# Optimization experiments

Measured on AMD Instinct MI355X. Metric: run time of the kernel, lower is better.

## Reference

```python
import jax, jax.numpy as jnp
import numpy as np

B, N, FIN, FOUT = 8, 4096, 64, 64
NEG_SLOPE = 0.01  # torch LeakyReLU default


def setup_inputs() -> dict:
    key = jax.random.key(0)
    k1, k2, k3, k4, k5 = jax.random.split(key, 5)
    inp = jax.random.normal(k1, (B, N, FIN), dtype=jnp.float32)
    adj = jax.random.randint(k2, (N, N), 0, 2, dtype=jnp.int32)
    W_w = jax.random.normal(k3, (FOUT, FIN), dtype=jnp.float32) * (1.0 / np.sqrt(FIN))
    W_b = jax.random.normal(k4, (FOUT,), dtype=jnp.float32) * 0.01
    a = jax.random.normal(k5, (2 * FOUT, N), dtype=jnp.float32) * (1.414 / np.sqrt(2 * FOUT + N))
    return {"inp": inp, "adj": adj, "W_w": W_w, "W_b": W_b, "a": a}


def reference(inp, adj, W_w, W_b, a):
    # h = W(inp); h[:, 0, :] = 0
    h = jnp.einsum('bnf,of->bno', inp, W_w) + W_b          # [B, N, F]
    h = h.at[:, 0, :].set(0.0)

    # Original loop: for i in 1..N-1:
    #   ac = a[:, i]  (shape [2F, 1])
    #   index = where(adj[1:, i] > 0)  -> 0-based, used to index h directly (bug preserved)
    #   s_i = h[:, i, :] @ ac[:F] + sum_j h[:, index, :] @ ac[F:]   (scalar per batch)
    #   attention[:, i, :] = s_i broadcast over all columns
    # Empty-index case equals the general case since an empty neighbor sum is 0.
    mask = (adj[1:, :] > 0).astype(h.dtype)                # [N-1, N]
    neigh = jnp.einsum('ji,bjf->bif', mask, h[:, :N - 1, :])  # [B, N, F]
    s = (jnp.einsum('bif,fi->bi', h, a[:FOUT]) +
         jnp.einsum('bif,fi->bi', neigh, a[FOUT:]))        # [B, N]
    s = s.at[:, 0].set(0.0)                                # attention row 0 stays zero

    # h_prime = attention @ h, with attention[b,i,j] = s[b,i] for all j
    hsum = h.sum(axis=1)                                   # [B, F]
    h_prime = s[:, :, None] * hsum[:, None, :]             # [B, N, F]
    return jnp.where(h_prime >= 0, h_prime, NEG_SLOPE * h_prime)
```

## Files before the change

kernel.cpp:

```cpp
#include <hip/hip_runtime.h>
#include <hip/hip_bf16.h>

#define NN 4096

typedef unsigned short u16;
typedef __attribute__((ext_vector_type(8))) short short8;
typedef __attribute__((ext_vector_type(4))) float f32x4;
typedef __attribute__((ext_vector_type(4))) unsigned short u16x4;
typedef __attribute__((ext_vector_type(8))) unsigned short u16x8;
typedef __attribute__((ext_vector_type(4))) int i32x4;

typedef const void __attribute__((address_space(1)))* gas_t;
typedef void __attribute__((address_space(3)))* las_t;

__device__ __forceinline__ u16 f2bf(float x) {
  unsigned u = __float_as_uint(x);
  return (u16)((u + 0x7FFFu + ((u >> 16) & 1)) >> 16);
}

__global__ __launch_bounds__(256) void k_maskT(const int* __restrict__ adj, u16* __restrict__ maskT) {
  __shared__ __align__(16) u16 tile[128 * 132];
  const int i0 = blockIdx.x * 128, j0 = blockIdx.y * 128;
  const int t = threadIdx.x;
  const int jr = t >> 5;
  const int il = t & 31;
#pragma unroll
  for (int pass = 0; pass < 16; ++pass) {
    const int jl = pass * 8 + jr;
    const int j = j0 + jl;
    u16 q[4] = {0, 0, 0, 0};
    if (j < NN - 1) {
      i32x4 av = *reinterpret_cast<const i32x4*>(&adj[(size_t)(j + 1) * NN + i0 + il * 4]);
      q[0] = av.x > 0 ? 0x3F80 : 0;
      q[1] = av.y > 0 ? 0x3F80 : 0;
      q[2] = av.z > 0 ? 0x3F80 : 0;
      q[3] = av.w > 0 ? 0x3F80 : 0;
    }
    const int pb = il ^ (jl >> 2);
    *reinterpret_cast<u16x4*>(&tile[jl * 132 + pb * 4]) = *reinterpret_cast<u16x4*>(q);
  }
  __syncthreads();
#pragma unroll
  for (int pass = 0; pass < 16; ++pass) {
    const int ir = pass * 8 + jr;
    const int ci = ir >> 2, io = ir & 3;
    u16 o[4];
#pragma unroll
    for (int d = 0; d < 4; ++d) {
      const int r = il * 4 + d;
      o[d] = tile[r * 132 + ((ci ^ il) << 2) + io];
    }
    *reinterpret_cast<u16x4*>(&maskT[(size_t)(i0 + ir) * NN + j0 + il * 4]) =
        *reinterpret_cast<u16x4*>(o);
  }
}

__global__ __launch_bounds__(256) void k_h(const float* __restrict__ inp, const float* __restrict__ Ww,
                                           const float* __restrict__ Wb, float* __restrict__ h,
                                           u16* __restrict__ h2t, float* __restrict__ hsum) {
  __shared__ __align__(16) u16 lA[128 * 64];
  __shared__ __align__(16) u16 lW[64 * 64];
  const int t = threadIdx.x, lane = t & 63, w = t >> 6;
  const int bid = blockIdx.x;
  const int b = bid >> 5;
  const size_t row0 = (size_t)bid * 128;
  {
    const int o = t >> 2, k0 = (t & 3) * 16;
    const float* src = &Ww[o * 64 + k0];
    u16 tmp[16];
#pragma unroll
    for (int e = 0; e < 16; ++e) tmp[e] = f2bf(src[e]);
    const int swz = (o & 7) * 8;
#pragma unroll
    for (int v = 0; v < 2; ++v)
      *reinterpret_cast<u16x8*>(&lW[o * 64 + ((k0 + v * 8) ^ swz)]) = *reinterpret_cast<u16x8*>(&tmp[v * 8]);
  }
  {
    const int r = t >> 1, k0 = (t & 1) * 32;
    const float* src = &inp[(row0 + r) * 64 + k0];
    u16 tmp[32];
#pragma unroll
    for (int e = 0; e < 32; ++e) tmp[e] = f2bf(src[e]);
    const int swz = (r & 7) * 8;
#pragma unroll
    for (int v = 0; v < 4; ++v)
      *reinterpret_cast<u16x8*>(&lA[r * 64 + ((k0 + v * 8) ^ swz)]) = *reinterpret_cast<u16x8*>(&tmp[v * 8]);
  }
  __syncthreads();
  f32x4 acc[2][4] = {};
#pragma unroll
  for (int ks = 0; ks < 2; ++ks) {
    const int kk = ks * 32 + (lane >> 4) * 8;
    short8 af[2], bf[4];
#pragma unroll
    for (int m = 0; m < 2; ++m) {
      const int row = w * 32 + m * 16 + (lane & 15);
      af[m] = *reinterpret_cast<const short8*>(&lA[row * 64 + (kk ^ ((row & 7) * 8))]);
    }
#pragma unroll
    for (int n = 0; n < 4; ++n) {
      const int o = n * 16 + (lane & 15);
      bf[n] = *reinterpret_cast<const short8*>(&lW[o * 64 + (kk ^ ((o & 7) * 8))]);
    }
#pragma unroll
    for (int m = 0; m < 2; ++m)
#pragma unroll
      for (int n = 0; n < 4; ++n)
        acc[m][n] = __builtin_amdgcn_mfma_f32_16x16x32_bf16(af[m], bf[n], acc[m][n], 0, 0, 0);
  }
  const int f0 = lane & 15;
  const int rsub = (lane >> 4) * 4;
  float wb[4];
#pragma unroll
  for (int n = 0; n < 4; ++n) wb[n] = Wb[n * 16 + f0];
  const int nloc_base = (bid & 31) * 128;
  float ps[4] = {0.f, 0.f, 0.f, 0.f};
#pragma unroll
  for (int m = 0; m < 2; ++m) {
    const int rl = w * 32 + m * 16 + rsub;
#pragma unroll
    for (int n = 0; n < 4; ++n) {
      u16 hb[4];
#pragma unroll
      for (int r = 0; r < 4; ++r) {
        float v = acc[m][n][r] + wb[n];
        if (nloc_base + rl + r == 0) v = 0.f;
        h[(row0 + rl + r) * 64 + n * 16 + f0] = v;
        hb[r] = f2bf(v);
        ps[n] += v;
      }
      *reinterpret_cast<u16x4*>(&h2t[(size_t)(b * 64 + n * 16 + f0) * NN + nloc_base + rl]) =
          *reinterpret_cast<u16x4*>(&hb[0]);
    }
  }
#pragma unroll
  for (int n = 0; n < 4; ++n) {
    float v = ps[n];
    v += __shfl_xor(v, 16);
    v += __shfl_xor(v, 32);
    if (lane < 16) atomicAdd(&hsum[b * 64 + n * 16 + f0], v);
  }
}

__global__ __launch_bounds__(256, 2) void k_gemm(const u16* __restrict__ A, const u16* __restrict__ Bm,
                                                 const float* __restrict__ a, float* __restrict__ s) {
  __shared__ __align__(16) u16 lA0[128 * 64], lA1[128 * 64];
  __shared__ __align__(16) u16 lB0[128 * 64], lB1[128 * 64];
  const int sid = blockIdx.x;
  const int wgid = (sid & 7) * 64 + (sid >> 3);
  const int c0 = (wgid & 3) * 128;
  const int i0 = ((wgid >> 2) & 31) * 128;
  const int z = wgid >> 7;
  const int t = threadIdx.x, lane = t & 63, w = t >> 6;
  const int wr = w >> 1, wc = w & 1;

  const int srow = lane >> 3;
  const int sk = ((lane & 7) ^ srow) * 8;
  const size_t kbase = (size_t)z * 1024;
  const u16* gA = A + (size_t)(i0 + w * 32 + srow) * NN + kbase + sk;
  const u16* gB = Bm + (size_t)(c0 + w * 32 + srow) * NN + kbase + sk;

#define STAGE_K(dstA, dstB, kt)                                                              \
  do {                                                                                       \
    _Pragma("unroll") for (int c = 0; c < 4; ++c) {                                          \
      __builtin_amdgcn_global_load_lds((gas_t)(gA + (size_t)(8 * c) * NN + (kt)),            \
                                       (las_t)((dstA) + (w * 32 + 8 * c) * 128 + lane * 16), \
                                       16, 0, 0);                                            \
      __builtin_amdgcn_global_load_lds((gas_t)(gB + (size_t)(8 * c) * NN + (kt)),            \
                                       (las_t)((dstB) + (w * 32 + 8 * c) * 128 + lane * 16), \
                                       16, 0, 0);                                            \
    }                                                                                        \
  } while (0)

  f32x4 acc[4][4] = {};
  asm volatile("" ::: "memory");
  STAGE_K((char*)lA0, (char*)lB0, 0);
#pragma unroll 1
  for (int it = 0; it < 16; ++it) {
    char* nA = (it & 1) ? (char*)lA0 : (char*)lA1;
    char* nB = (it & 1) ? (char*)lB0 : (char*)lB1;
    if (it < 15) {
      STAGE_K(nA, nB, (it + 1) * 64);
      asm volatile("s_waitcnt vmcnt(8)" ::: "memory");
    } else {
      asm volatile("s_waitcnt vmcnt(0)" ::: "memory");
    }
    __builtin_amdgcn_s_barrier();
    asm volatile("" ::: "memory");
    const u16* cA = (it & 1) ? lA1 : lA0;
    const u16* cB = (it & 1) ? lB1 : lB0;
#pragma unroll
    for (int ks = 0; ks < 2; ++ks) {
      const int kb = ks * 4 + (lane >> 4);
      short8 af[4], bfr[4];
#pragma unroll
      for (int m = 0; m < 4; ++m) {
        const int row = wr * 64 + m * 16 + (lane & 15);
        af[m] = *reinterpret_cast<const short8*>(&cA[row * 64 + ((kb ^ (row & 7)) * 8)]);
      }
#pragma unroll
      for (int n = 0; n < 4; ++n) {
        const int row = wc * 64 + n * 16 + (lane & 15);
        bfr[n] = *reinterpret_cast<const short8*>(&cB[row * 64 + ((kb ^ (row & 7)) * 8)]);
      }
#pragma unroll
      for (int m = 0; m < 4; ++m)
#pragma unroll
        for (int n = 0; n < 4; ++n)
          acc[m][n] = __builtin_amdgcn_mfma_f32_16x16x32_bf16(af[m], bfr[n], acc[m][n], 0, 0, 0);
    }
    asm volatile("" ::: "memory");
    __builtin_amdgcn_s_barrier();
  }
#undef STAGE_K
  const int b = (c0 >> 7) * 2 + wc;
  const int f0 = lane & 15, rsub = (lane >> 4) * 4;
  float pp[4][4];
#pragma unroll
  for (int m = 0; m < 4; ++m) {
    const int irow = i0 + wr * 64 + m * 16 + rsub;
#pragma unroll
    for (int r = 0; r < 4; ++r) pp[m][r] = 0.f;
#pragma unroll
    for (int n = 0; n < 4; ++n) {
      f32x4 a2v = *reinterpret_cast<const f32x4*>(&a[(size_t)(64 + n * 16 + f0) * NN + irow]);
#pragma unroll
      for (int r = 0; r < 4; ++r) pp[m][r] += acc[m][n][r] * a2v[r];
    }
  }
#pragma unroll
  for (int m = 0; m < 4; ++m)
#pragma unroll
    for (int r = 0; r < 4; ++r) {
      float v = pp[m][r];
      v += __shfl_xor(v, 1);
      v += __shfl_xor(v, 2);
      v += __shfl_xor(v, 4);
      v += __shfl_xor(v, 8);
      pp[m][r] = v;
    }
  if (f0 == 0) {
    const int irow = i0 + wr * 64 + rsub;
#pragma unroll
    for (int m = 0; m < 4; ++m)
#pragma unroll
      for (int r = 0; r < 4; ++r)
        atomicAdd(&s[(size_t)b * NN + irow + m * 16 + r], pp[m][r]);
  }
}

__global__ __launch_bounds__(256) void k_final(const float* __restrict__ h, const float* __restrict__ sg,
                                               const float* __restrict__ a, const float* __restrict__ hsum,
                                               float* __restrict__ out) {
  __shared__ float a1[64][65];
  __shared__ float hs[64], sv[64];
  const int b = blockIdx.x >> 6;
  const int i0 = (blockIdx.x & 63) * 64;
  const int t = threadIdx.x;
  {
    const int lr = t >> 6, li = t & 63;
#pragma unroll
    for (int rr = 0; rr < 64; rr += 4)
      a1[rr + lr][li] = a[(size_t)(rr + lr) * NN + i0 + li];
    if (t < 64) hs[t] = hsum[b * 64 + t];
  }
  __syncthreads();
  const int il = t >> 2, q = t & 3;
  const int i = i0 + il;
  const float* hrow = &h[((size_t)b * NN + i) * 64 + q * 16];
  float p = 0.f;
#pragma unroll
  for (int k = 0; k < 16; ++k) p += hrow[k] * a1[q * 16 + k][il];
  p += __shfl_down(p, 2, 4);
  p += __shfl_down(p, 1, 4);
  if (q == 0) sv[il] = (i == 0) ? 0.f : (p + sg[(size_t)b * NN + i]);
  __syncthreads();
  const int lf = t & 63, lr2 = t >> 6;
#pragma unroll
  for (int rr = 0; rr < 64; rr += 4) {
    int ii = rr + lr2;
    float val = sv[ii] * hs[lf];
    out[((size_t)b * NN + i0 + ii) * 64 + lf] = (val >= 0.f) ? val : 0.01f * val;
  }
}

extern "C" void kernel_launch(void* const* d_in, const int* in_sizes, int n_in,
                              void* d_out, int out_size, void* d_ws, size_t ws_size,
                              hipStream_t stream) {
  const float* inp = (const float*)d_in[0];
  const int* adj = (const int*)d_in[1];
  const float* Ww = (const float*)d_in[2];
  const float* Wb = (const float*)d_in[3];
  const float* a = (const float*)d_in[4];
  float* out = (float*)d_out;
  char* ws = (char*)d_ws;

  float* s = (float*)ws;
  float* hsum = (float*)(ws + 131072);
  u16* maskT = (u16*)(ws + 262144);
  u16* h2t = (u16*)(ws + 262144 + 33554432);
  float* h = (float*)(ws + 262144 + 33554432 + 4194304);

  hipMemsetAsync(ws, 0, 133120, stream);
  hipLaunchKernelGGL(k_maskT, dim3(32, 32), dim3(256), 0, stream, adj, maskT);
  hipLaunchKernelGGL(k_h, dim3(256), dim3(256), 0, stream, inp, Ww, Wb, h, h2t, hsum);
  hipLaunchKernelGGL(k_gemm, dim3(512), dim3(256), 0, stream, maskT, h2t, a, s);
  hipLaunchKernelGGL(k_final, dim3(512), dim3(256), 0, stream, h, s, a, hsum, out);
}
```

Measured before the change: 153.1 us.

## Fuse mask transpose and h projection into one prep kernel, drop fp32 h buffer

Merges the adjacency transpose and the h projection into a single launch split by block index, and drops the memset and one kernel launch. The self-attention term h·a1 now runs in the projection epilogue, so the fp32 h buffer is no longer written or read back. hsum atomics become per-block partials that k_final reduces, and s is zeroed inside the prep kernel. k_final now stores float4 vectors. The trade-off is an extra strided read of a inside the prep epilogue and a redundant partial reduction in every final block.

Result: no change. 153.6 us (+0.3%).

```diff
diff --git a/kernel.cpp b/kernel.cpp
--- a/kernel.cpp
+++ b/kernel.cpp
@@ -18,52 +18,60 @@
   return (u16)((u + 0x7FFFu + ((u >> 16) & 1)) >> 16);
 }
 
-__global__ __launch_bounds__(256) void k_maskT(const int* __restrict__ adj, u16* __restrict__ maskT) {
-  __shared__ __align__(16) u16 tile[128 * 132];
-  const int i0 = blockIdx.x * 128, j0 = blockIdx.y * 128;
+__global__ __launch_bounds__(256) void k_prep(const int* __restrict__ adj, const float* __restrict__ inp,
+                                              const float* __restrict__ Ww, const float* __restrict__ Wb,
+                                              const float* __restrict__ a, u16* __restrict__ maskT,
+                                              u16* __restrict__ h2t, float* __restrict__ p1,
+                                              float* __restrict__ hpart, float* __restrict__ s) {
+  __shared__ __align__(16) char Lraw[33792];
+  __shared__ float wsum[4][64];
+  const int bid = blockIdx.x;
   const int t = threadIdx.x;
-  const int jr = t >> 5;
-  const int il = t & 31;
-#pragma unroll
-  for (int pass = 0; pass < 16; ++pass) {
-    const int jl = pass * 8 + jr;
-    const int j = j0 + jl;
-    u16 q[4] = {0, 0, 0, 0};
-    if (j < NN - 1) {
-      i32x4 av = *reinterpret_cast<const i32x4*>(&adj[(size_t)(j + 1) * NN + i0 + il * 4]);
-      q[0] = av.x > 0 ? 0x3F80 : 0;
-      q[1] = av.y > 0 ? 0x3F80 : 0;
-      q[2] = av.z > 0 ? 0x3F80 : 0;
-      q[3] = av.w > 0 ? 0x3F80 : 0;
-    }
-    const int pb = il ^ (jl >> 2);
-    *reinterpret_cast<u16x4*>(&tile[jl * 132 + pb * 4]) = *reinterpret_cast<u16x4*>(q);
-  }
-  __syncthreads();
-#pragma unroll
-  for (int pass = 0; pass < 16; ++pass) {
-    const int ir = pass * 8 + jr;
-    const int ci = ir >> 2, io = ir & 3;
-    u16 o[4];
-#pragma unroll
-    for (int d = 0; d < 4; ++d) {
-      const int r = il * 4 + d;
-      o[d] = tile[r * 132 + ((ci ^ il) << 2) + io];
-    }
-    *reinterpret_cast<u16x4*>(&maskT[(size_t)(i0 + ir) * NN + j0 + il * 4]) =
-        *reinterpret_cast<u16x4*>(o);
-  }
-}
-
-__global__ __launch_bounds__(256) void k_h(const float* __restrict__ inp, const float* __restrict__ Ww,
-                                           const float* __restrict__ Wb, float* __restrict__ h,
-                                           u16* __restrict__ h2t, float* __restrict__ hsum) {
-  __shared__ __align__(16) u16 lA[128 * 64];
-  __shared__ __align__(16) u16 lW[64 * 64];
-  const int t = threadIdx.x, lane = t & 63, w = t >> 6;
-  const int bid = blockIdx.x;
-  const int b = bid >> 5;
-  const size_t row0 = (size_t)bid * 128;
+
+  if (bid < 1024) {
+    u16* tile = (u16*)Lraw;
+    const int i0 = (bid & 31) * 128, j0 = (bid >> 5) * 128;
+    const int jr = t >> 5;
+    const int il = t & 31;
+#pragma unroll
+    for (int pass = 0; pass < 16; ++pass) {
+      const int jl = pass * 8 + jr;
+      const int j = j0 + jl;
+      u16 q[4] = {0, 0, 0, 0};
+      if (j < NN - 1) {
+        i32x4 av = *reinterpret_cast<const i32x4*>(&adj[(size_t)(j + 1) * NN + i0 + il * 4]);
+        q[0] = av.x > 0 ? 0x3F80 : 0;
+        q[1] = av.y > 0 ? 0x3F80 : 0;
+        q[2] = av.z > 0 ? 0x3F80 : 0;
+        q[3] = av.w > 0 ? 0x3F80 : 0;
+      }
+      const int pb = il ^ (jl >> 2);
+      *reinterpret_cast<u16x4*>(&tile[jl * 132 + pb * 4]) = *reinterpret_cast<u16x4*>(q);
+    }
+    __syncthreads();
+#pragma unroll
+    for (int pass = 0; pass < 16; ++pass) {
+      const int ir = pass * 8 + jr;
+      const int ci = ir >> 2, io = ir & 3;
+      u16 o[4];
+#pragma unroll
+      for (int d = 0; d < 4; ++d) {
+        const int r = il * 4 + d;
+        o[d] = tile[r * 132 + ((ci ^ il) << 2) + io];
+      }
+      *reinterpret_cast<u16x4*>(&maskT[(size_t)(i0 + ir) * NN + j0 + il * 4]) =
+          *reinterpret_cast<u16x4*>(o);
+    }
+    return;
+  }
+
+  u16* lA = (u16*)Lraw;
+  u16* lW = (u16*)(Lraw + 16384);
+  const int hb = bid - 1024;
+  const int lane = t & 63, w = t >> 6;
+  const int b = hb >> 5;
+  const size_t row0 = (size_t)hb * 128;
+  if (t < 128) s[hb * 128 + t] = 0.f;
   {
     const int o = t >> 2, k0 = (t & 3) * 16;
     const float* src = &Ww[o * 64 + k0];
@@ -113,24 +121,37 @@
   float wb[4];
 #pragma unroll
   for (int n = 0; n < 4; ++n) wb[n] = Wb[n * 16 + f0];
-  const int nloc_base = (bid & 31) * 128;
+  const int nloc_base = (hb & 31) * 128;
   float ps[4] = {0.f, 0.f, 0.f, 0.f};
 #pragma unroll
   for (int m = 0; m < 2; ++m) {
     const int rl = w * 32 + m * 16 + rsub;
+    float vz[4][4];
 #pragma unroll
     for (int n = 0; n < 4; ++n) {
-      u16 hb[4];
+      u16 hb4[4];
 #pragma unroll
       for (int r = 0; r < 4; ++r) {
         float v = acc[m][n][r] + wb[n];
         if (nloc_base + rl + r == 0) v = 0.f;
-        h[(row0 + rl + r) * 64 + n * 16 + f0] = v;
-        hb[r] = f2bf(v);
+        vz[n][r] = v;
+        hb4[r] = f2bf(v);
         ps[n] += v;
       }
       *reinterpret_cast<u16x4*>(&h2t[(size_t)(b * 64 + n * 16 + f0) * NN + nloc_base + rl]) =
-          *reinterpret_cast<u16x4*>(&hb[0]);
+          *reinterpret_cast<u16x4*>(&hb4[0]);
+    }
+#pragma unroll
+    for (int r = 0; r < 4; ++r) {
+      const int ig = nloc_base + rl + r;
+      float pv = 0.f;
+#pragma unroll
+      for (int n = 0; n < 4; ++n) pv += vz[n][r] * a[(size_t)(n * 16 + f0) * NN + ig];
+      pv += __shfl_xor(pv, 1);
+      pv += __shfl_xor(pv, 2);
+      pv += __shfl_xor(pv, 4);
+      pv += __shfl_xor(pv, 8);
+      if (f0 == 0) p1[(size_t)b * NN + ig] = pv;
     }
   }
 #pragma unroll
@@ -138,8 +159,10 @@
     float v = ps[n];
     v += __shfl_xor(v, 16);
     v += __shfl_xor(v, 32);
-    if (lane < 16) atomicAdd(&hsum[b * 64 + n * 16 + f0], v);
-  }
+    if (lane < 16) wsum[w][n * 16 + f0] = v;
+  }
+  __syncthreads();
+  if (t < 64) hpart[hb * 64 + t] = wsum[0][t] + wsum[1][t] + wsum[2][t] + wsum[3][t];
 }
 
 __global__ __launch_bounds__(256, 2) void k_gemm(const u16* __restrict__ A, const u16* __restrict__ Bm,
@@ -249,38 +272,39 @@
   }
 }
 
-__global__ __launch_bounds__(256) void k_final(const float* __restrict__ h, const float* __restrict__ sg,
-                                               const float* __restrict__ a, const float* __restrict__ hsum,
-                                               float* __restrict__ out) {
-  __shared__ float a1[64][65];
+__global__ __launch_bounds__(256) void k_final(const float* __restrict__ p1, const float* __restrict__ sg,
+                                               const float* __restrict__ hpart, float* __restrict__ out) {
+  __shared__ float hp[4][64];
   __shared__ float hs[64], sv[64];
   const int b = blockIdx.x >> 6;
   const int i0 = (blockIdx.x & 63) * 64;
   const int t = threadIdx.x;
   {
-    const int lr = t >> 6, li = t & 63;
-#pragma unroll
-    for (int rr = 0; rr < 64; rr += 4)
-      a1[rr + lr][li] = a[(size_t)(rr + lr) * NN + i0 + li];
-    if (t < 64) hs[t] = hsum[b * 64 + t];
+    const int f = t & 63, g = t >> 6;
+    float acc = 0.f;
+#pragma unroll
+    for (int sl = 0; sl < 8; ++sl) acc += hpart[(size_t)(b * 32 + g * 8 + sl) * 64 + f];
+    hp[g][f] = acc;
   }
   __syncthreads();
-  const int il = t >> 2, q = t & 3;
-  const int i = i0 + il;
-  const float* hrow = &h[((size_t)b * NN + i) * 64 + q * 16];
-  float p = 0.f;
-#pragma unroll
-  for (int k = 0; k < 16; ++k) p += hrow[k] * a1[q * 16 + k][il];
-  p += __shfl_down(p, 2, 4);
-  p += __shfl_down(p, 1, 4);
-  if (q == 0) sv[il] = (i == 0) ? 0.f : (p + sg[(size_t)b * NN + i]);
+  if (t < 64) {
+    hs[t] = hp[0][t] + hp[1][t] + hp[2][t] + hp[3][t];
+    const int i = i0 + t;
+    sv[t] = (i == 0) ? 0.f : (p1[(size_t)b * NN + i] + sg[(size_t)b * NN + i]);
+  }
   __syncthreads();
-  const int lf = t & 63, lr2 = t >> 6;
-#pragma unroll
-  for (int rr = 0; rr < 64; rr += 4) {
-    int ii = rr + lr2;
-    float val = sv[ii] * hs[lf];
-    out[((size_t)b * NN + i0 + ii) * 64 + lf] = (val >= 0.f) ? val : 0.01f * val;
+  const int fq = (t & 15) * 4, ir = t >> 4;
+#pragma unroll
+  for (int pass = 0; pass < 4; ++pass) {
+    const int ii = pass * 16 + ir;
+    const float svi = sv[ii];
+    f32x4 o;
+#pragma unroll
+    for (int k = 0; k < 4; ++k) {
+      float val = svi * hs[fq + k];
+      o[k] = (val >= 0.f) ? val : 0.01f * val;
+    }
+    *reinterpret_cast<f32x4*>(&out[((size_t)b * NN + i0 + ii) * 64 + fq]) = o;
   }
 }
 
@@ -296,14 +320,13 @@
   char* ws = (char*)d_ws;
 
   float* s = (float*)ws;
-  float* hsum = (float*)(ws + 131072);
-  u16* maskT = (u16*)(ws + 262144);
-  u16* h2t = (u16*)(ws + 262144 + 33554432);
-  float* h = (float*)(ws + 262144 + 33554432 + 4194304);
-
-  hipMemsetAsync(ws, 0, 133120, stream);
-  hipLaunchKernelGGL(k_maskT, dim3(32, 32), dim3(256), 0, stream, adj, maskT);
-  hipLaunchKernelGGL(k_h, dim3(256), dim3(256), 0, stream, inp, Ww, Wb, h, h2t, hsum);
+  float* hpart = (float*)(ws + 131072);
+  float* p1 = (float*)(ws + 196608);
+  u16* maskT = (u16*)(ws + 524288);
+  u16* h2t = (u16*)(ws + 524288 + 33554432);
+
+  hipLaunchKernelGGL(k_prep, dim3(1280), dim3(256), 0, stream, adj, inp, Ww, Wb, a,
+                     maskT, h2t, p1, hpart, s);
   hipLaunchKernelGGL(k_gemm, dim3(512), dim3(256), 0, stream, maskT, h2t, a, s);
-  hipLaunchKernelGGL(k_final, dim3(512), dim3(256), 0, stream, h, s, a, hsum, out);
-}
+  hipLaunchKernelGGL(k_final, dim3(512), dim3(256), 0, stream, p1, s, hpart, out);
+}
```
